# Kernel optimization log

Hardware: AMD Instinct MI355X
Metric: run time of the kernel (lower is better)

## Reference

```python
import jax, jax.numpy as jnp
import numpy as np

LEAKY = 0.01   # torch LeakyReLU default negative_slope
BN_EPS = 1e-5  # torch BatchNorm1d default eps


def _batchnorm(x, gamma, beta):
    # train-mode BatchNorm1d: normalize with per-batch biased statistics
    mean = jnp.mean(x, axis=0)
    var = jnp.var(x, axis=0)
    return (x - mean) * jax.lax.rsqrt(var + BN_EPS) * gamma + beta


def setup_inputs() -> dict:
    key = jax.random.key(0)
    ks = jax.random.split(key, 8)
    B, F, depth = 32768, 1, 10
    n_nodes = 2 ** depth  # 1024
    x = jax.random.normal(ks[0], (B, F), jnp.float32)
    prenet_w1 = jax.random.normal(ks[1], (16, F), jnp.float32) * 0.5
    prenet_b1 = jax.random.normal(ks[2], (16,), jnp.float32) * 0.1
    bn1_gamma = jnp.ones((16,), jnp.float32)
    bn1_beta = jnp.zeros((16,), jnp.float32)
    prenet_w2 = jax.random.normal(ks[3], (F, 16), jnp.float32) * 0.25
    prenet_b2 = jax.random.normal(ks[4], (F,), jnp.float32) * 0.1
    bn2_gamma = jnp.ones((F,), jnp.float32)
    bn2_beta = jnp.zeros((F,), jnp.float32)
    fc_w = jax.random.normal(ks[5], (n_nodes, F, F), jnp.float32) * 0.5
    fc_b = jax.random.normal(ks[6], (n_nodes, F), jnp.float32) * 0.1
    return {
        'x': x,
        'prenet_w1': prenet_w1, 'prenet_b1': prenet_b1,
        'bn1_gamma': bn1_gamma, 'bn1_beta': bn1_beta,
        'prenet_w2': prenet_w2, 'prenet_b2': prenet_b2,
        'bn2_gamma': bn2_gamma, 'bn2_beta': bn2_beta,
        'fc_w': fc_w, 'fc_b': fc_b,
    }


def reference(x, prenet_w1, prenet_b1, bn1_gamma, bn1_beta,
              prenet_w2, prenet_b2, bn2_gamma, bn2_beta, fc_w, fc_b):
    # prenet: Linear -> LeakyReLU -> BN -> Linear -> LeakyReLU -> BN
    h = jax.nn.leaky_relu(x @ prenet_w1.T + prenet_b1, LEAKY)
    h = _batchnorm(h, bn1_gamma, bn1_beta)
    h = jax.nn.leaky_relu(h @ prenet_w2.T + prenet_b2, LEAKY)
    x = _batchnorm(h, bn2_gamma, bn2_beta)

    # per-node Linear + sigmoid, fused as one batched GEMM:
    # (B,F) x (n_nodes,F,F) -> (B, n_nodes, F); here F == 1
    d = jax.nn.sigmoid(jnp.einsum('bf,nof->bno', x, fc_w) + fc_b)
    decision = jnp.concatenate([d, 1.0 - d], axis=2)  # (B, n_nodes, 2)

    B = x.shape[0]
    depth = int(np.log2(fc_w.shape[0]))
    mu = jnp.ones((B, 2, 1), x.dtype)
    begin, end = 1, 2
    for n_layer in range(depth):  # small fixed loop over tree depth
        # route parent probs to both children: (B, 2^n, 2)
        nu = jnp.tile(mu[:, begin:, :], (1, 1, 2)) * decision[:, begin:end, :]
        begin, end = end, end + 2 ** (n_layer + 1)
        mu = jnp.concatenate([mu, nu.reshape(B, -1, 1)], axis=1)
    mu = mu[..., 0]           # (B, 2^(depth+1))
    return mu.at[:, 0].set(0.0)
```

## Files before the change

### kernel.cpp

```cpp
#include <hip/hip_runtime.h>

#define LEAKY_S 0.01f
#define BN_EPS 1e-5f
#define LOG2E 1.44269504088896340736f

typedef float f32x2 __attribute__((ext_vector_type(2)));
typedef float f32x4 __attribute__((ext_vector_type(4)));

__device__ __forceinline__ float leaky(float v) { return v >= 0.0f ? v : LEAKY_S * v; }
__device__ __forceinline__ float fast_exp2(float v) { return __builtin_amdgcn_exp2f(v); }
__device__ __forceinline__ float sig2(float z2) {
    return __builtin_amdgcn_rcpf(1.0f + fast_exp2(-z2));
}
__device__ __forceinline__ void st2(float* p, float a, float b) {
    f32x2 v = {a, b}; *(f32x2*)p = v;
}
__device__ __forceinline__ void st_nt2(float* p, float a, float b) {
    f32x2 v = {a, b}; __builtin_nontemporal_store(v, (f32x2*)p);
}
__device__ __forceinline__ void st_nt4(float* p, float a, float b, float c, float d) {
    f32x4 v = {a, b, c, d}; __builtin_nontemporal_store(v, (f32x4*)p);
}

__global__ __launch_bounds__(256) void k_part1(const float* __restrict__ x,
        const float* __restrict__ w1, const float* __restrict__ b1,
        float* __restrict__ p1, int B) {
    float w1r[16], b1r[16], s[16], q[16];
#pragma unroll
    for (int j = 0; j < 16; ++j) { w1r[j] = w1[j]; b1r[j] = b1[j]; s[j] = 0.f; q[j] = 0.f; }
    int tid = threadIdx.x;
    int i = blockIdx.x * 256 + tid;
    if (2 * i < B) {
        f32x2 xv = *(const f32x2*)(x + 2 * i);
#pragma unroll
        for (int e = 0; e < 2; ++e) {
#pragma unroll
            for (int j = 0; j < 16; ++j) {
                float h = leaky(fmaf(xv[e], w1r[j], b1r[j]));
                s[j] += h; q[j] += h * h;
            }
        }
    }
#pragma unroll
    for (int j = 0; j < 16; ++j) {
        for (int off = 32; off >= 1; off >>= 1) {
            s[j] += __shfl_xor(s[j], off, 64);
            q[j] += __shfl_xor(q[j], off, 64);
        }
    }
    __shared__ float red[4][32];
    int w = tid >> 6, lane = tid & 63;
    if (lane == 0) {
#pragma unroll
        for (int j = 0; j < 16; ++j) { red[w][j] = s[j]; red[w][j + 16] = q[j]; }
    }
    __syncthreads();
    if (tid < 32)
        p1[blockIdx.x * 32 + tid] = red[0][tid] + red[1][tid] + red[2][tid] + red[3][tid];
}

__device__ __forceinline__ void fold_bn1(const float* __restrict__ p1,
        const float* __restrict__ w2, const float* __restrict__ b2,
        const float* __restrict__ g1, const float* __restrict__ be1,
        float* coef, int tid, float invB) {
    float acc = 0.f;
    for (int i = 0; i < 64; ++i) acc += p1[i * 32 + tid];
    float qacc = __shfl(acc, tid + 16, 64);
    float cp = 0.f;
    if (tid < 16) {
        float mean = acc * invB;
        float var  = qacc * invB - mean * mean;
        float inv  = rsqrtf(var + BN_EPS) * g1[tid];
        float sh   = fmaf(-mean, inv, be1[tid]);
        coef[tid] = inv * w2[tid];
        cp = sh * w2[tid];
    }
    for (int off = 8; off >= 1; off >>= 1) cp += __shfl_xor(cp, off, 16);
    if (tid == 0) coef[16] = cp + b2[0];
}

__global__ __launch_bounds__(256) void k_h2f(const float* __restrict__ x,
        const float* __restrict__ w1, const float* __restrict__ b1,
        const float* __restrict__ p1, const float* __restrict__ w2,
        const float* __restrict__ b2, const float* __restrict__ g1,
        const float* __restrict__ be1, float* __restrict__ p2,
        float* __restrict__ cfws, int B, float invB) {
    __shared__ float coef[17];
    int tid = threadIdx.x;
    if (tid < 32) fold_bn1(p1, w2, b2, g1, be1, coef, tid, invB);
    __syncthreads();
    if (blockIdx.x == 0 && tid < 17) cfws[tid] = coef[tid];
    float w1r[16], b1r[16], ar[16];
#pragma unroll
    for (int j = 0; j < 16; ++j) { w1r[j] = w1[j]; b1r[j] = b1[j]; ar[j] = coef[j]; }
    float c0 = coef[16];
    float s = 0.f, q = 0.f;
    int i = blockIdx.x * 256 + tid;
    if (2 * i < B) {
        f32x2 xv = *(const f32x2*)(x + 2 * i);
#pragma unroll
        for (int e = 0; e < 2; ++e) {
            float acc = c0;
#pragma unroll
            for (int j = 0; j < 16; ++j) {
                float h = leaky(fmaf(xv[e], w1r[j], b1r[j]));
                acc = fmaf(h, ar[j], acc);
            }
            float h2 = leaky(acc);
            s += h2; q += h2 * h2;
        }
    }
    for (int off = 32; off >= 1; off >>= 1) {
        s += __shfl_xor(s, off, 64);
        q += __shfl_xor(q, off, 64);
    }
    __shared__ float red[4][2];
    int w = tid >> 6, lane = tid & 63;
    if (lane == 0) { red[w][0] = s; red[w][1] = q; }
    __syncthreads();
    if (tid == 0) {
        p2[blockIdx.x * 2 + 0] = red[0][0] + red[1][0] + red[2][0] + red[3][0];
        p2[blockIdx.x * 2 + 1] = red[0][1] + red[1][1] + red[2][1] + red[3][1];
    }
}

__global__ __launch_bounds__(256) void k_tree(const float* __restrict__ x,
        const float* __restrict__ w1, const float* __restrict__ b1,
        const float* __restrict__ g2, const float* __restrict__ be2,
        const float* __restrict__ fcw, const float* __restrict__ fcb,
        const float* __restrict__ p2, const float* __restrict__ cfws,
        float* __restrict__ out, int B, float invB) {
    __shared__ float wl[1024], bl[1024];
    __shared__ float x2s[32];
    __shared__ float bn2[2];
    int tid = threadIdx.x;

    for (int i = tid; i < 1024; i += 256) {
        int d;
        if (i < 128)      d = i;
        else if (i < 256) { int o = i - 128; d = 128 + ((o & 1) << 6) + (o >> 1); }
        else if (i < 512) { int o = i - 256; d = 256 + ((((o >> 7) << 1) | (o & 1)) << 6) + ((o & 127) >> 1); }
        else              { int o = i - 512; d = 512 + ((((o >> 7) << 1) | (o & 1)) << 6) + ((o & 127) >> 1); }
        wl[d] = fcw[i];
        bl[d] = fcb[i];
    }
    if (tid < 64) {
        float s = p2[2 * tid], q = p2[2 * tid + 1];
        for (int off = 32; off >= 1; off >>= 1) {
            s += __shfl_xor(s, off, 64);
            q += __shfl_xor(q, off, 64);
        }
        if (tid == 0) {
            float mean = s * invB, var = q * invB - mean * mean;
            float inv = rsqrtf(var + BN_EPS) * g2[0];
            bn2[0] = inv;
            bn2[1] = fmaf(-mean, inv, be2[0]);
        }
    }
    __syncthreads();
    {
        float s2k = bn2[0] * LOG2E, t2 = bn2[1];
        for (int i = tid; i < 1024; i += 256) {
            float wv = wl[i];
            wl[i] = wv * s2k;
            bl[i] = fmaf(t2, wv, bl[i]) * LOG2E;
        }
    }
    if (tid < 32) {
        int r = blockIdx.x * 32 + tid;
        float xv = (r < B) ? x[r] : 0.f;
        float acc = cfws[16];
#pragma unroll
        for (int j = 0; j < 16; ++j) {
            float h = leaky(fmaf(xv, w1[j], b1[j]));
            acc = fmaf(h, cfws[j], acc);
        }
        x2s[tid] = leaky(acc);
    }
    __syncthreads();

    const int w = tid >> 6, lane = tid & 63;
    const int rbase = blockIdx.x * 32 + w * 8;
    for (int rp = 0; rp < 4; ++rp) {
        const int r0 = rbase + 2 * rp;
        float x2[2]; bool act[2]; float* op[2];
#pragma unroll
        for (int rr = 0; rr < 2; ++rr) {
            x2[rr] = x2s[w * 8 + 2 * rp + rr];
            act[rr] = (r0 + rr) < B;
            op[rr] = out + (size_t)(r0 + rr) * 2048;
            if (act[rr] && lane == 0) st2(op[rr], 0.f, 1.f);
        }

        float mup[2] = {1.f, 1.f};
#pragma unroll
        for (int l = 1; l <= 6; ++l) {
            const int P = 1 << (l - 1);
            float wv = wl[P + lane], bv = bl[P + lane];
#pragma unroll
            for (int rr = 0; rr < 2; ++rr) {
                float z = fmaf(x2[rr], wv, bv);
                float pz = sig2(z);
                float c0 = mup[rr] * pz, c1 = mup[rr] - c0;
                if (act[rr] && lane < P) {
                    if (l >= 5) st_nt2(op[rr] + 2 * (P + lane), c0, c1);
                    else        st2(op[rr] + 2 * (P + lane), c0, c1);
                }
                float s0 = __shfl(c0, lane >> 1, 64);
                float s1 = __shfl(c1, lane >> 1, 64);
                mup[rr] = (lane & 1) ? s1 : s0;
            }
        }
        float c2[2][2];
        {
            float wv = wl[64 + lane], bv = bl[64 + lane];
#pragma unroll
            for (int rr = 0; rr < 2; ++rr) {
                float z = fmaf(x2[rr], wv, bv);
                float pz = sig2(z);
                c2[rr][0] = mup[rr] * pz;
                c2[rr][1] = mup[rr] - c2[rr][0];
                if (act[rr]) st_nt2(op[rr] + 128 + 2 * lane, c2[rr][0], c2[rr][1]);
            }
        }
        float c4[2][4];
#pragma unroll
        for (int s = 0; s < 2; ++s) {
            float wv = wl[128 + (s << 6) + lane], bv = bl[128 + (s << 6) + lane];
#pragma unroll
            for (int rr = 0; rr < 2; ++rr) {
                float z = fmaf(x2[rr], wv, bv);
                float pz = sig2(z);
                c4[rr][2 * s]     = c2[rr][s] * pz;
                c4[rr][2 * s + 1] = c2[rr][s] - c4[rr][2 * s];
            }
        }
#pragma unroll
        for (int rr = 0; rr < 2; ++rr)
            if (act[rr])
                st_nt4(op[rr] + 256 + (lane << 2), c4[rr][0], c4[rr][1], c4[rr][2], c4[rr][3]);
        float c8[2][2][4];
#pragma unroll
        for (int j2 = 0; j2 < 2; ++j2) {
            int src = (j2 << 5) + (lane >> 1);
            float wv0 = wl[256 + ((2 * j2) << 6) + lane],     bv0 = bl[256 + ((2 * j2) << 6) + lane];
            float wv1 = wl[256 + ((2 * j2 + 1) << 6) + lane], bv1 = bl[256 + ((2 * j2 + 1) << 6) + lane];
#pragma unroll
            for (int rr = 0; rr < 2; ++rr) {
                float A  = __shfl(c4[rr][0], src, 64);
                float Bv = __shfl(c4[rr][1], src, 64);
                float C  = __shfl(c4[rr][2], src, 64);
                float D  = __shfl(c4[rr][3], src, 64);
                float m0 = (lane & 1) ? C : A;
                float m1 = (lane & 1) ? D : Bv;
                float z0 = fmaf(x2[rr], wv0, bv0);
                float z1 = fmaf(x2[rr], wv1, bv1);
                float p0 = sig2(z0), p1v = sig2(z1);
                c8[rr][j2][0] = m0 * p0;
                c8[rr][j2][1] = m0 - c8[rr][j2][0];
                c8[rr][j2][2] = m1 * p1v;
                c8[rr][j2][3] = m1 - c8[rr][j2][2];
                if (act[rr])
                    st_nt4(op[rr] + 512 + (j2 << 8) + (lane << 2),
                           c8[rr][j2][0], c8[rr][j2][1], c8[rr][j2][2], c8[rr][j2][3]);
            }
        }
#pragma unroll
        for (int j = 0; j < 4; ++j) {
            const int j2 = j >> 1;
            int src = ((j & 1) << 5) + (lane >> 1);
            float wv0 = wl[512 + ((2 * j) << 6) + lane],     bv0 = bl[512 + ((2 * j) << 6) + lane];
            float wv1 = wl[512 + ((2 * j + 1) << 6) + lane], bv1 = bl[512 + ((2 * j + 1) << 6) + lane];
#pragma unroll
            for (int rr = 0; rr < 2; ++rr) {
                float A  = __shfl(c8[rr][j2][0], src, 64);
                float Bv = __shfl(c8[rr][j2][1], src, 64);
                float C  = __shfl(c8[rr][j2][2], src, 64);
                float D  = __shfl(c8[rr][j2][3], src, 64);
                float m0 = (lane & 1) ? C : A;
                float m1 = (lane & 1) ? D : Bv;
                float z0 = fmaf(x2[rr], wv0, bv0);
                float z1 = fmaf(x2[rr], wv1, bv1);
                float p0 = sig2(z0), p1v = sig2(z1);
                float a0 = m0 * p0,  a1 = m0 - a0;
                float b0 = m1 * p1v, b1 = m1 - b0;
                if (act[rr])
                    st_nt4(op[rr] + 1024 + (j << 8) + (lane << 2), a0, a1, b0, b1);
            }
        }
    }
}

extern "C" void kernel_launch(void* const* d_in, const int* in_sizes, int n_in,
                              void* d_out, int out_size, void* d_ws, size_t ws_size,
                              hipStream_t stream) {
    const float* x   = (const float*)d_in[0];
    const float* w1  = (const float*)d_in[1];
    const float* b1  = (const float*)d_in[2];
    const float* g1  = (const float*)d_in[3];
    const float* be1 = (const float*)d_in[4];
    const float* w2  = (const float*)d_in[5];
    const float* b2  = (const float*)d_in[6];
    const float* g2  = (const float*)d_in[7];
    const float* be2 = (const float*)d_in[8];
    const float* fcw = (const float*)d_in[9];
    const float* fcb = (const float*)d_in[10];
    float* out = (float*)d_out;
    int B = in_sizes[0];
    float invB = 1.0f / (float)B;

    float* ws = (float*)d_ws;
    float* p1 = ws;
    float* p2 = ws + 2048;
    float* cf = ws + 2176;

    k_part1<<<64, 256, 0, stream>>>(x, w1, b1, p1, B);
    k_h2f  <<<64, 256, 0, stream>>>(x, w1, b1, p1, w2, b2, g1, be1, p2, cf, B, invB);

    int blocks = (B + 31) / 32;
    k_tree<<<blocks, 256, 0, stream>>>(x, w1, b1, g2, be2, fcw, fcb, p2, cf,
                                       out, B, invB);
}
```

Before: 66.48 us.

## Assign one row per wavefront with four rows per block in tree kernel

The tree kernel now gives each 64-lane wavefront a single batch row, so a 256-thread block covers 4 rows and the grid grows eightfold. Before, each wave looped over 8 rows two at a time. The x2 prenet evaluation moves before the first barrier, handled by threads 64-67 while wave 0 reduces the BN2 statistics. The aim is more parallelism and more memory-level concurrency for the output stores. In exchange, every block repeats the 1024-entry weight/bias load, permutation and rescale, and that setup is now spread over far fewer rows per block.

New measurement: 64.62 us. -2.8%, faster.

```diff
diff --git a/kernel.cpp b/kernel.cpp
--- a/kernel.cpp
+++ b/kernel.cpp
@@ -131,7 +131,7 @@
         const float* __restrict__ p2, const float* __restrict__ cfws,
         float* __restrict__ out, int B, float invB) {
     __shared__ float wl[1024], bl[1024];
-    __shared__ float x2s[32];
+    __shared__ float x2s[4];
     __shared__ float bn2[2];
     int tid = threadIdx.x;
 
@@ -157,6 +157,18 @@
             bn2[1] = fmaf(-mean, inv, be2[0]);
         }
     }
+    if (tid >= 64 && tid < 68) {
+        int rr = tid - 64;
+        int r = blockIdx.x * 4 + rr;
+        float xv = (r < B) ? x[r] : 0.f;
+        float acc = cfws[16];
+#pragma unroll
+        for (int j = 0; j < 16; ++j) {
+            float h = leaky(fmaf(xv, w1[j], b1[j]));
+            acc = fmaf(h, cfws[j], acc);
+        }
+        x2s[rr] = leaky(acc);
+    }
     __syncthreads();
     {
         float s2k = bn2[0] * LOG2E, t2 = bn2[1];
@@ -166,128 +178,93 @@
             bl[i] = fmaf(t2, wv, bl[i]) * LOG2E;
         }
     }
-    if (tid < 32) {
-        int r = blockIdx.x * 32 + tid;
-        float xv = (r < B) ? x[r] : 0.f;
-        float acc = cfws[16];
-#pragma unroll
-        for (int j = 0; j < 16; ++j) {
-            float h = leaky(fmaf(xv, w1[j], b1[j]));
-            acc = fmaf(h, cfws[j], acc);
-        }
-        x2s[tid] = leaky(acc);
-    }
     __syncthreads();
 
     const int w = tid >> 6, lane = tid & 63;
-    const int rbase = blockIdx.x * 32 + w * 8;
-    for (int rp = 0; rp < 4; ++rp) {
-        const int r0 = rbase + 2 * rp;
-        float x2[2]; bool act[2]; float* op[2];
-#pragma unroll
-        for (int rr = 0; rr < 2; ++rr) {
-            x2[rr] = x2s[w * 8 + 2 * rp + rr];
-            act[rr] = (r0 + rr) < B;
-            op[rr] = out + (size_t)(r0 + rr) * 2048;
-            if (act[rr] && lane == 0) st2(op[rr], 0.f, 1.f);
-        }
-
-        float mup[2] = {1.f, 1.f};
-#pragma unroll
-        for (int l = 1; l <= 6; ++l) {
-            const int P = 1 << (l - 1);
-            float wv = wl[P + lane], bv = bl[P + lane];
-#pragma unroll
-            for (int rr = 0; rr < 2; ++rr) {
-                float z = fmaf(x2[rr], wv, bv);
-                float pz = sig2(z);
-                float c0 = mup[rr] * pz, c1 = mup[rr] - c0;
-                if (act[rr] && lane < P) {
-                    if (l >= 5) st_nt2(op[rr] + 2 * (P + lane), c0, c1);
-                    else        st2(op[rr] + 2 * (P + lane), c0, c1);
-                }
-                float s0 = __shfl(c0, lane >> 1, 64);
-                float s1 = __shfl(c1, lane >> 1, 64);
-                mup[rr] = (lane & 1) ? s1 : s0;
-            }
-        }
-        float c2[2][2];
-        {
-            float wv = wl[64 + lane], bv = bl[64 + lane];
-#pragma unroll
-            for (int rr = 0; rr < 2; ++rr) {
-                float z = fmaf(x2[rr], wv, bv);
-                float pz = sig2(z);
-                c2[rr][0] = mup[rr] * pz;
-                c2[rr][1] = mup[rr] - c2[rr][0];
-                if (act[rr]) st_nt2(op[rr] + 128 + 2 * lane, c2[rr][0], c2[rr][1]);
-            }
-        }
-        float c4[2][4];
-#pragma unroll
-        for (int s = 0; s < 2; ++s) {
-            float wv = wl[128 + (s << 6) + lane], bv = bl[128 + (s << 6) + lane];
-#pragma unroll
-            for (int rr = 0; rr < 2; ++rr) {
-                float z = fmaf(x2[rr], wv, bv);
-                float pz = sig2(z);
-                c4[rr][2 * s]     = c2[rr][s] * pz;
-                c4[rr][2 * s + 1] = c2[rr][s] - c4[rr][2 * s];
-            }
-        }
-#pragma unroll
-        for (int rr = 0; rr < 2; ++rr)
-            if (act[rr])
-                st_nt4(op[rr] + 256 + (lane << 2), c4[rr][0], c4[rr][1], c4[rr][2], c4[rr][3]);
-        float c8[2][2][4];
-#pragma unroll
-        for (int j2 = 0; j2 < 2; ++j2) {
-            int src = (j2 << 5) + (lane >> 1);
-            float wv0 = wl[256 + ((2 * j2) << 6) + lane],     bv0 = bl[256 + ((2 * j2) << 6) + lane];
-            float wv1 = wl[256 + ((2 * j2 + 1) << 6) + lane], bv1 = bl[256 + ((2 * j2 + 1) << 6) + lane];
-#pragma unroll
-            for (int rr = 0; rr < 2; ++rr) {
-                float A  = __shfl(c4[rr][0], src, 64);
-                float Bv = __shfl(c4[rr][1], src, 64);
-                float C  = __shfl(c4[rr][2], src, 64);
-                float D  = __shfl(c4[rr][3], src, 64);
-                float m0 = (lane & 1) ? C : A;
-                float m1 = (lane & 1) ? D : Bv;
-                float z0 = fmaf(x2[rr], wv0, bv0);
-                float z1 = fmaf(x2[rr], wv1, bv1);
-                float p0 = sig2(z0), p1v = sig2(z1);
-                c8[rr][j2][0] = m0 * p0;
-                c8[rr][j2][1] = m0 - c8[rr][j2][0];
-                c8[rr][j2][2] = m1 * p1v;
-                c8[rr][j2][3] = m1 - c8[rr][j2][2];
-                if (act[rr])
-                    st_nt4(op[rr] + 512 + (j2 << 8) + (lane << 2),
-                           c8[rr][j2][0], c8[rr][j2][1], c8[rr][j2][2], c8[rr][j2][3]);
-            }
-        }
-#pragma unroll
-        for (int j = 0; j < 4; ++j) {
-            const int j2 = j >> 1;
-            int src = ((j & 1) << 5) + (lane >> 1);
-            float wv0 = wl[512 + ((2 * j) << 6) + lane],     bv0 = bl[512 + ((2 * j) << 6) + lane];
-            float wv1 = wl[512 + ((2 * j + 1) << 6) + lane], bv1 = bl[512 + ((2 * j + 1) << 6) + lane];
-#pragma unroll
-            for (int rr = 0; rr < 2; ++rr) {
-                float A  = __shfl(c8[rr][j2][0], src, 64);
-                float Bv = __shfl(c8[rr][j2][1], src, 64);
-                float C  = __shfl(c8[rr][j2][2], src, 64);
-                float D  = __shfl(c8[rr][j2][3], src, 64);
-                float m0 = (lane & 1) ? C : A;
-                float m1 = (lane & 1) ? D : Bv;
-                float z0 = fmaf(x2[rr], wv0, bv0);
-                float z1 = fmaf(x2[rr], wv1, bv1);
-                float p0 = sig2(z0), p1v = sig2(z1);
-                float a0 = m0 * p0,  a1 = m0 - a0;
-                float b0 = m1 * p1v, b1 = m1 - b0;
-                if (act[rr])
-                    st_nt4(op[rr] + 1024 + (j << 8) + (lane << 2), a0, a1, b0, b1);
-            }
-        }
+    const int r = blockIdx.x * 4 + w;
+    const bool act = r < B;
+    const float x2 = x2s[w];
+    float* op = out + (size_t)r * 2048;
+    if (act && lane == 0) st2(op, 0.f, 1.f);
+
+    float mup = 1.f;
+#pragma unroll
+    for (int l = 1; l <= 6; ++l) {
+        const int P = 1 << (l - 1);
+        float wv = wl[P + lane], bv = bl[P + lane];
+        float z = fmaf(x2, wv, bv);
+        float pz = sig2(z);
+        float c0 = mup * pz, c1 = mup - c0;
+        if (act && lane < P) {
+            if (l >= 5) st_nt2(op + 2 * (P + lane), c0, c1);
+            else        st2(op + 2 * (P + lane), c0, c1);
+        }
+        float s0 = __shfl(c0, lane >> 1, 64);
+        float s1 = __shfl(c1, lane >> 1, 64);
+        mup = (lane & 1) ? s1 : s0;
+    }
+    float c2v[2];
+    {
+        float wv = wl[64 + lane], bv = bl[64 + lane];
+        float z = fmaf(x2, wv, bv);
+        float pz = sig2(z);
+        c2v[0] = mup * pz;
+        c2v[1] = mup - c2v[0];
+        if (act) st_nt2(op + 128 + 2 * lane, c2v[0], c2v[1]);
+    }
+    float c4v[4];
+#pragma unroll
+    for (int s = 0; s < 2; ++s) {
+        float wv = wl[128 + (s << 6) + lane], bv = bl[128 + (s << 6) + lane];
+        float z = fmaf(x2, wv, bv);
+        float pz = sig2(z);
+        c4v[2 * s]     = c2v[s] * pz;
+        c4v[2 * s + 1] = c2v[s] - c4v[2 * s];
+    }
+    if (act)
+        st_nt4(op + 256 + (lane << 2), c4v[0], c4v[1], c4v[2], c4v[3]);
+    float c8v[2][4];
+#pragma unroll
+    for (int j2 = 0; j2 < 2; ++j2) {
+        int src = (j2 << 5) + (lane >> 1);
+        float A  = __shfl(c4v[0], src, 64);
+        float Bv = __shfl(c4v[1], src, 64);
+        float C  = __shfl(c4v[2], src, 64);
+        float D  = __shfl(c4v[3], src, 64);
+        float m0 = (lane & 1) ? C : A;
+        float m1 = (lane & 1) ? D : Bv;
+        float wv0 = wl[256 + ((2 * j2) << 6) + lane],     bv0 = bl[256 + ((2 * j2) << 6) + lane];
+        float wv1 = wl[256 + ((2 * j2 + 1) << 6) + lane], bv1 = bl[256 + ((2 * j2 + 1) << 6) + lane];
+        float z0 = fmaf(x2, wv0, bv0);
+        float z1 = fmaf(x2, wv1, bv1);
+        float p0 = sig2(z0), p1v = sig2(z1);
+        c8v[j2][0] = m0 * p0;
+        c8v[j2][1] = m0 - c8v[j2][0];
+        c8v[j2][2] = m1 * p1v;
+        c8v[j2][3] = m1 - c8v[j2][2];
+        if (act)
+            st_nt4(op + 512 + (j2 << 8) + (lane << 2),
+                   c8v[j2][0], c8v[j2][1], c8v[j2][2], c8v[j2][3]);
+    }
+#pragma unroll
+    for (int j = 0; j < 4; ++j) {
+        const int j2 = j >> 1;
+        int src = ((j & 1) << 5) + (lane >> 1);
+        float A  = __shfl(c8v[j2][0], src, 64);
+        float Bv = __shfl(c8v[j2][1], src, 64);
+        float C  = __shfl(c8v[j2][2], src, 64);
+        float D  = __shfl(c8v[j2][3], src, 64);
+        float m0 = (lane & 1) ? C : A;
+        float m1 = (lane & 1) ? D : Bv;
+        float wv0 = wl[512 + ((2 * j) << 6) + lane],     bv0 = bl[512 + ((2 * j) << 6) + lane];
+        float wv1 = wl[512 + ((2 * j + 1) << 6) + lane], bv1 = bl[512 + ((2 * j + 1) << 6) + lane];
+        float z0 = fmaf(x2, wv0, bv0);
+        float z1 = fmaf(x2, wv1, bv1);
+        float p0 = sig2(z0), p1v = sig2(z1);
+        float a0 = m0 * p0,  a1 = m0 - a0;
+        float b0 = m1 * p1v, b1 = m1 - b0;
+        if (act)
+            st_nt4(op + 1024 + (j << 8) + (lane << 2), a0, a1, b0, b1);
     }
 }
 
@@ -317,7 +294,7 @@
     k_part1<<<64, 256, 0, stream>>>(x, w1, b1, p1, B);
     k_h2f  <<<64, 256, 0, stream>>>(x, w1, b1, p1, w2, b2, g1, be1, p2, cf, B, invB);
 
-    int blocks = (B + 31) / 32;
+    int blocks = (B + 3) / 4;
     k_tree<<<blocks, 256, 0, stream>>>(x, w1, b1, g2, be2, fcw, fcb, p2, cf,
                                        out, B, invB);
 }
```
